# Kernel optimization log

Measured on AMD Instinct MI355X. Metric: run time of the kernel, lower is better.

The kernel has to match this reference:

```python
import jax, jax.numpy as jnp
import numpy as np

B, N, D, H = 8, 2048, 256, 8
HD = D // H  # head_dim = 32
LN_EPS = 1e-5


def setup_inputs() -> dict:
    key = jax.random.key(0)
    ks = jax.random.split(key, 8)
    x = jax.random.normal(ks[0], (B, N, D), dtype=jnp.float32)
    # dense 0/1 adjacency with guaranteed self-loops (avoids all -inf softmax rows)
    adj = jax.random.randint(ks[1], (B, N, N), 0, 2, dtype=jnp.int32)
    adj = jnp.maximum(adj, jnp.eye(N, dtype=jnp.int32)[None, :, :])
    s = 0.02
    Wq = jax.random.normal(ks[2], (D, D), dtype=jnp.float32) * s
    Wk = jax.random.normal(ks[3], (D, D), dtype=jnp.float32) * s
    Wv = jax.random.normal(ks[4], (D, D), dtype=jnp.float32) * s
    Wo = jax.random.normal(ks[5], (D, D), dtype=jnp.float32) * s
    zeros = jnp.zeros((D,), dtype=jnp.float32)
    return {
        "x": x, "adjacency": adj,
        "Wq": Wq, "bq": zeros, "Wk": Wk, "bk": zeros,
        "Wv": Wv, "bv": zeros, "Wo": Wo, "bo": zeros,
        "gamma": jnp.ones((D,), dtype=jnp.float32), "beta": zeros,
    }


def reference(x, adjacency, Wq, bq, Wk, bk, Wv, bv, Wo, bo, gamma, beta):
    b, n, d = x.shape
    q = (x @ Wq + bq).reshape(b, n, H, HD)
    k = (x @ Wk + bk).reshape(b, n, H, HD)
    v = (x @ Wv + bv).reshape(b, n, H, HD)
    # scores: [B, N(query), M(key), H]
    scores = jnp.einsum('bnhd,bmhd->bnmh', q, k) / jnp.sqrt(jnp.float32(HD))
    mask = (adjacency == 0)[..., None]  # [B,N,M,1] broadcasts over heads
    scores = jnp.where(mask, -jnp.inf, scores)
    weights = jax.nn.softmax(scores, axis=2)  # softmax over key axis m
    # dropout is identity in eval mode
    attended = jnp.einsum('bnmh,bmhd->bnhd', weights, v).reshape(b, n, d)
    out = attended @ Wo + bo
    out = out + x  # residual (output.shape == x.shape since input_dim == output_dim)
    mu = jnp.mean(out, axis=-1, keepdims=True)
    var = jnp.mean(jnp.square(out - mu), axis=-1, keepdims=True)
    return (out - mu) * jax.lax.rsqrt(var + LN_EPS) * gamma + beta
```

## Files before the change

### kernel.cpp

```cpp
#include <hip/hip_runtime.h>
#include <hip/hip_bf16.h>
#include <cstdint>
#include <cstddef>

#define B_ 8
#define N_ 2048
#define D_ 256
#define H_ 8
#define HD_ 32
#define LN_EPS 1e-5f
#define QSCALE 0.25506275f

typedef __attribute__((ext_vector_type(8))) short short8;
typedef __attribute__((ext_vector_type(4))) float f32x4;
typedef __attribute__((ext_vector_type(16))) float f32x16;

static __device__ __forceinline__ float exp2v(float x) {
#if __has_builtin(__builtin_amdgcn_exp2f)
    return __builtin_amdgcn_exp2f(x);
#else
    float r;
    asm("v_exp_f32 %0, %1" : "=v"(r) : "v"(x));
    return r;
#endif
}

static __device__ __forceinline__ unsigned short f2bf(float f) {
    union { float f; unsigned int u; } v; v.f = f;
    unsigned int r = v.u + 0x7fffu + ((v.u >> 16) & 1u);
    return (unsigned short)(r >> 16);
}

static __device__ __forceinline__ float bf2f(unsigned short u) {
    union { unsigned int u; float f; } v; v.u = ((unsigned int)u) << 16;
    return v.f;
}

static __device__ __forceinline__ unsigned int cvtpk(float lo, float hi) {
    unsigned int d;
    asm("v_cvt_pk_bf16_f32 %0, %1, %2" : "=v"(d) : "v"(lo), "v"(hi));
    return d;
}

__global__ __launch_bounds__(256) void k_prep_x(const float* __restrict__ x,
                                                unsigned short* __restrict__ xbf, int n4) {
    int i = blockIdx.x * 256 + threadIdx.x;
    if (i >= n4) return;
    float4 v = reinterpret_cast<const float4*>(x)[i];
    ushort4 o;
    o.x = f2bf(v.x); o.y = f2bf(v.y); o.z = f2bf(v.z); o.w = f2bf(v.w);
    reinterpret_cast<ushort4*>(xbf)[i] = o;
}

__global__ __launch_bounds__(256) void k_prep_w(const float* __restrict__ w0, const float* __restrict__ w1,
                                                const float* __restrict__ w2, const float* __restrict__ w3,
                                                unsigned short* __restrict__ wt) {
    int c = blockIdx.x, mat = blockIdx.y, k = threadIdx.x;
    const float* w = (mat == 0) ? w0 : (mat == 1) ? w1 : (mat == 2) ? w2 : w3;
    wt[((size_t)(mat * 256 + c)) * 256 + k] = f2bf(w[k * 256 + c]);
}

__global__ __launch_bounds__(256) void k_mask(const int* __restrict__ adj,
                                              unsigned int* __restrict__ mbg) {
    int wave = (blockIdx.x * 256 + threadIdx.x) >> 6;
    int lane = threadIdx.x & 63;
    int shamt = 4 * (lane & 7);
    int g8 = lane >> 3;
    const int4* p = reinterpret_cast<const int4*>(adj) + (size_t)wave * 1024 + lane;
    unsigned int* outp = mbg + (size_t)wave * 128;

    int4 v[16];
#pragma unroll
    for (int i = 0; i < 16; ++i)
        v[i] = p[i * 64];

#pragma unroll
    for (int i = 0; i < 16; ++i) {
        unsigned int nib = (v[i].x != 0 ? 1u : 0u) | (v[i].y != 0 ? 2u : 0u)
                         | (v[i].z != 0 ? 4u : 0u) | (v[i].w != 0 ? 8u : 0u);
        unsigned int r = nib << shamt;
        r |= (unsigned int)__shfl_xor((int)r, 1, 64);
        r |= (unsigned int)__shfl_xor((int)r, 2, 64);
        r |= (unsigned int)__shfl_xor((int)r, 4, 64);
        if ((lane & 7) == 0) outp[i * 8 + g8] = r;
    }
}

__global__ __launch_bounds__(256) void k_qkv(const unsigned short* __restrict__ xbf,
                                             const unsigned short* __restrict__ wt,
                                             const float* __restrict__ bq, const float* __restrict__ bk,
                                             const float* __restrict__ bv,
                                             unsigned short* __restrict__ Qb, unsigned short* __restrict__ Kb,
                                             unsigned short* __restrict__ Vs) {
    int mat = blockIdx.y;
    int lane = threadIdx.x & 63;
    int wv = threadIdx.x >> 6;
    int row0 = blockIdx.x * 64 + wv * 16;
    int l15 = lane & 15, lg = lane >> 4;
    const float* bias = (mat == 0) ? bq : (mat == 1) ? bk : bv;
    const float qs = (mat == 0) ? QSCALE : 1.0f;
    const unsigned short* wm = wt + (size_t)mat * 65536;

    short8 af[8];
    const unsigned short* xrow = xbf + (size_t)(row0 + l15) * 256 + lg * 8;
#pragma unroll
    for (int kk = 0; kk < 8; ++kk)
        af[kk] = *reinterpret_cast<const short8*>(xrow + kk * 32);

    int b = row0 >> 11;
    int nbase = (row0 & 2047) + lg * 4;

    for (int ci = 0; ci < 16; ++ci) {
        const unsigned short* wrow = wm + (size_t)(ci * 16 + l15) * 256 + lg * 8;
        f32x4 acc = {0.f, 0.f, 0.f, 0.f};
#pragma unroll
        for (int kk = 0; kk < 8; ++kk) {
            short8 bfg = *reinterpret_cast<const short8*>(wrow + kk * 32);
            acc = __builtin_amdgcn_mfma_f32_16x16x32_bf16(af[kk], bfg, acc, 0, 0, 0);
        }
        int col = ci * 16 + l15;
        float bcol = bias[col];
        int h = col >> 5, hd = col & 31;
        if (mat < 2) {
            unsigned short* dst = (mat == 0) ? Qb : Kb;
#pragma unroll
            for (int r = 0; r < 4; ++r) {
                size_t off = ((size_t)(b * 8 + h) * 2048 + nbase + r) * 32 + hd;
                dst[off] = f2bf((acc[r] + bcol) * qs);
            }
        } else {
            size_t off = (size_t)(b * 8 + h) * 65536
                       + ((size_t)(nbase >> 4) * 32 + hd) * 16 + (nbase & 15);
            ushort4 o;
            o.x = f2bf(acc[0] + bcol); o.y = f2bf(acc[1] + bcol);
            o.z = f2bf(acc[2] + bcol); o.w = f2bf(acc[3] + bcol);
            *reinterpret_cast<ushort4*>(Vs + off) = o;
        }
    }
}

__global__ __launch_bounds__(256, 6) void k_attn(const unsigned short* __restrict__ Qb,
                                                 const unsigned short* __restrict__ Kb,
                                                 const unsigned short* __restrict__ Vs,
                                                 const unsigned int* __restrict__ mbg,
                                                 unsigned short* __restrict__ att) {
    __shared__ unsigned int mbits[32][66];
    int tid = threadIdx.x;
    int lane = tid & 63;
    int l31 = lane & 31, hi = lane >> 5;
    int b = blockIdx.x & 7;
    int hg = (blockIdx.x >> 3) & 1;
    int q0 = (blockIdx.x >> 4) * 32;
    int head = hg * 4 + (tid >> 6);

    {
        int row = tid >> 3, c0 = (tid & 7) * 8;
        const unsigned int* src = mbg + ((size_t)(b * N_ + q0 + row)) * 64 + c0;
        uint4 v4 = *reinterpret_cast<const uint4*>(src);
        uint4 w4 = *reinterpret_cast<const uint4*>(src + 4);
        mbits[row][c0 + 0] = v4.x; mbits[row][c0 + 1] = v4.y;
        mbits[row][c0 + 2] = v4.z; mbits[row][c0 + 3] = v4.w;
        mbits[row][c0 + 4] = w4.x; mbits[row][c0 + 5] = w4.y;
        mbits[row][c0 + 6] = w4.z; mbits[row][c0 + 7] = w4.w;
    }
    __syncthreads();

    int bh = b * 8 + head;
    const unsigned short* Qh = Qb + (size_t)bh * N_ * HD_;
    const unsigned short* Kh = Kb + (size_t)bh * N_ * HD_;
    const unsigned short* Vh = Vs + (size_t)bh * 65536;

    short8 qf0 = *reinterpret_cast<const short8*>(Qh + (size_t)(q0 + l31) * HD_ + hi * 8);
    short8 qf1 = *reinterpret_cast<const short8*>(Qh + (size_t)(q0 + l31) * HD_ + hi * 8 + 16);
    const unsigned short* krow = Kh + (size_t)l31 * HD_ + hi * 8;
    const unsigned short* vfp = Vh + (size_t)l31 * 16 + hi * 8;

    const f32x16 fz = {0.f,0.f,0.f,0.f,0.f,0.f,0.f,0.f,0.f,0.f,0.f,0.f,0.f,0.f,0.f,0.f};
    const short8 onesf = {0x3F80, 0x3F80, 0x3F80, 0x3F80, 0x3F80, 0x3F80, 0x3F80, 0x3F80};
    f32x16 attacc = fz;
    f32x16 onesacc = fz;
    const unsigned int* mrow = &mbits[l31][0];

#pragma unroll 2
    for (int m0 = 0; m0 < N_; m0 += 32) {
        short8 kf0 = *reinterpret_cast<const short8*>(krow + (size_t)m0 * HD_);
        short8 kf1 = *reinterpret_cast<const short8*>(krow + (size_t)m0 * HD_ + 16);
        short8 vf0 = *reinterpret_cast<const short8*>(vfp + (size_t)(m0 >> 4) * 512);
        short8 vf1 = *reinterpret_cast<const short8*>(vfp + (size_t)(m0 >> 4) * 512 + 512);
        unsigned int wl = mrow[m0 >> 5] >> (4 * hi);

        __builtin_amdgcn_s_setprio(1);
        f32x16 s = __builtin_amdgcn_mfma_f32_32x32x16_bf16(kf0, qf0, fz, 0, 0, 0);
        s = __builtin_amdgcn_mfma_f32_32x32x16_bf16(kf1, qf1, s, 0, 0, 0);
        __builtin_amdgcn_s_setprio(0);

        unsigned int pd[4][2];
#pragma unroll
        for (int g = 0; g < 4; ++g) {
            unsigned int nib = (wl >> (8 * g)) & 15u;
            float p0 = (nib & 1u) ? exp2v(s[4 * g + 0]) : 0.f;
            float p1 = (nib & 2u) ? exp2v(s[4 * g + 1]) : 0.f;
            float p2 = (nib & 4u) ? exp2v(s[4 * g + 2]) : 0.f;
            float p3 = (nib & 8u) ? exp2v(s[4 * g + 3]) : 0.f;
            pd[g][0] = cvtpk(p0, p1);
            pd[g][1] = cvtpk(p2, p3);
        }
        asm("v_permlane32_swap_b32 %0, %1" : "+v"(pd[0][0]), "+v"(pd[1][0]));
        asm("v_permlane32_swap_b32 %0, %1" : "+v"(pd[0][1]), "+v"(pd[1][1]));
        asm("v_permlane32_swap_b32 %0, %1" : "+v"(pd[2][0]), "+v"(pd[3][0]));
        asm("v_permlane32_swap_b32 %0, %1" : "+v"(pd[2][1]), "+v"(pd[3][1]));

        union { short8 s8; unsigned int u[4]; } bf0, bf1;
        bf0.u[0] = pd[0][0]; bf0.u[1] = pd[0][1]; bf0.u[2] = pd[1][0]; bf0.u[3] = pd[1][1];
        bf1.u[0] = pd[2][0]; bf1.u[1] = pd[2][1]; bf1.u[2] = pd[3][0]; bf1.u[3] = pd[3][1];

        __builtin_amdgcn_s_setprio(1);
        attacc = __builtin_amdgcn_mfma_f32_32x32x16_bf16(vf0, bf0.s8, attacc, 0, 0, 0);
        attacc = __builtin_amdgcn_mfma_f32_32x32x16_bf16(vf1, bf1.s8, attacc, 0, 0, 0);
        onesacc = __builtin_amdgcn_mfma_f32_32x32x16_bf16(onesf, bf0.s8, onesacc, 0, 0, 0);
        onesacc = __builtin_amdgcn_mfma_f32_32x32x16_bf16(onesf, bf1.s8, onesacc, 0, 0, 0);
        __builtin_amdgcn_s_setprio(0);
    }

    float rcp = 1.f / onesacc[0];

    unsigned short* arow = att + ((size_t)b * N_ + q0 + l31) * D_ + head * HD_;
#pragma unroll
    for (int g = 0; g < 4; ++g) {
        ushort4 o;
        o.x = f2bf(attacc[4 * g + 0] * rcp);
        o.y = f2bf(attacc[4 * g + 1] * rcp);
        o.z = f2bf(attacc[4 * g + 2] * rcp);
        o.w = f2bf(attacc[4 * g + 3] * rcp);
        *reinterpret_cast<ushort4*>(arow + 8 * g + 4 * hi) = o;
    }
}

__global__ __launch_bounds__(256) void k_outln(const unsigned short* __restrict__ att,
                                               const unsigned short* __restrict__ wot,
                                               const float* __restrict__ bo,
                                               const unsigned short* __restrict__ xbf,
                                               const float* __restrict__ gamma, const float* __restrict__ beta,
                                               float* __restrict__ out) {
    int lane = threadIdx.x & 63, wv = threadIdx.x >> 6;
    int l15 = lane & 15, lg = lane >> 4;
    int row0 = blockIdx.x * 64 + wv * 16;

    short8 af[8];
    const unsigned short* arow = att + (size_t)(row0 + l15) * 256 + lg * 8;
#pragma unroll
    for (int kk = 0; kk < 8; ++kk)
        af[kk] = *reinterpret_cast<const short8*>(arow + kk * 32);

    float v[16][4];
#pragma unroll
    for (int ci = 0; ci < 16; ++ci) {
        const unsigned short* wrow = wot + (size_t)(ci * 16 + l15) * 256 + lg * 8;
        f32x4 acc = {0.f, 0.f, 0.f, 0.f};
#pragma unroll
        for (int kk = 0; kk < 8; ++kk) {
            short8 bfg = *reinterpret_cast<const short8*>(wrow + kk * 32);
            acc = __builtin_amdgcn_mfma_f32_16x16x32_bf16(af[kk], bfg, acc, 0, 0, 0);
        }
        float bcol = bo[ci * 16 + l15];
#pragma unroll
        for (int r = 0; r < 4; ++r)
            v[ci][r] = acc[r] + bcol + bf2f(xbf[(size_t)(row0 + lg * 4 + r) * 256 + ci * 16 + l15]);
    }

    float sum[4] = {0.f, 0.f, 0.f, 0.f}, sq[4] = {0.f, 0.f, 0.f, 0.f};
#pragma unroll
    for (int ci = 0; ci < 16; ++ci)
#pragma unroll
        for (int r = 0; r < 4; ++r) {
            sum[r] += v[ci][r];
            sq[r] += v[ci][r] * v[ci][r];
        }
#pragma unroll
    for (int d = 1; d < 16; d <<= 1)
#pragma unroll
        for (int r = 0; r < 4; ++r) {
            sum[r] += __shfl_xor(sum[r], d, 64);
            sq[r] += __shfl_xor(sq[r], d, 64);
        }

    float mu[4], rs[4];
#pragma unroll
    for (int r = 0; r < 4; ++r) {
        mu[r] = sum[r] * (1.f / 256.f);
        float var = sq[r] * (1.f / 256.f) - mu[r] * mu[r];
        rs[r] = rsqrtf(var + LN_EPS);
    }

#pragma unroll
    for (int ci = 0; ci < 16; ++ci) {
        float g = gamma[ci * 16 + l15], be = beta[ci * 16 + l15];
#pragma unroll
        for (int r = 0; r < 4; ++r)
            out[(size_t)(row0 + lg * 4 + r) * 256 + ci * 16 + l15] = (v[ci][r] - mu[r]) * rs[r] * g + be;
    }
}

extern "C" void kernel_launch(void* const* d_in, const int* in_sizes, int n_in,
                              void* d_out, int out_size, void* d_ws, size_t ws_size,
                              hipStream_t stream) {
    (void)in_sizes; (void)n_in; (void)out_size; (void)ws_size;
    const float* x     = (const float*)d_in[0];
    const int*   adj   = (const int*)d_in[1];
    const float* Wq    = (const float*)d_in[2];
    const float* bq    = (const float*)d_in[3];
    const float* Wk    = (const float*)d_in[4];
    const float* bk    = (const float*)d_in[5];
    const float* Wv    = (const float*)d_in[6];
    const float* bv    = (const float*)d_in[7];
    const float* Wo    = (const float*)d_in[8];
    const float* bo    = (const float*)d_in[9];
    const float* gamma = (const float*)d_in[10];
    const float* beta  = (const float*)d_in[11];
    float* out = (float*)d_out;

    char* ws = (char*)d_ws;
    unsigned short* xbf = (unsigned short*)ws; ws += (size_t)16384 * 256 * 2;
    unsigned short* wt  = (unsigned short*)ws; ws += (size_t)4 * 256 * 256 * 2;
    unsigned short* Qb  = (unsigned short*)ws; ws += (size_t)B_ * H_ * N_ * HD_ * 2;
    unsigned short* Kb  = (unsigned short*)ws; ws += (size_t)B_ * H_ * N_ * HD_ * 2;
    unsigned short* Vs  = (unsigned short*)ws; ws += (size_t)B_ * H_ * N_ * HD_ * 2;
    unsigned short* att = (unsigned short*)ws; ws += (size_t)16384 * 256 * 2;
    unsigned int*   mbg = (unsigned int*)ws;   ws += (size_t)B_ * N_ * 64 * 4;

    k_prep_x<<<4096, 256, 0, stream>>>(x, xbf, 1048576);
    k_prep_w<<<dim3(256, 4), 256, 0, stream>>>(Wq, Wk, Wv, Wo, wt);
    k_mask<<<2048, 256, 0, stream>>>(adj, mbg);
    k_qkv<<<dim3(256, 3), 256, 0, stream>>>(xbf, wt, bq, bk, bv, Qb, Kb, Vs);
    k_attn<<<1024, 256, 0, stream>>>(Qb, Kb, Vs, mbg, att);
    k_outln<<<256, 256, 0, stream>>>(att, wt + 3 * 65536, bo, xbf, gamma, beta, out);
}
```

Measured before the change: 184.1 us.

## Share K/V tiles across four query waves via double-buffered LDS staging

Attention blocks now cover one (batch, head) with four waves over 128 queries, instead of four heads over 32 queries. Each 32-key K/V tile is loaded cooperatively into a double-buffered LDS buffer and reused by all four waves. K and V are written in a fragment-ready layout so each staging load is contiguous. The mask kernel now emits a transposed bitmask so each wave reads one coalesced word per key tile. The change trades a block-wide barrier every tile and lower occupancy (launch bounds 6 to 4) for fourfold less global K/V traffic. The mask kernel also launches far fewer blocks.

```diff
diff --git a/kernel.cpp b/kernel.cpp
--- a/kernel.cpp
+++ b/kernel.cpp
@@ -60,29 +60,44 @@
     wt[((size_t)(mat * 256 + c)) * 256 + k] = f2bf(w[k * 256 + c]);
 }
 
-__global__ __launch_bounds__(256) void k_mask(const int* __restrict__ adj,
-                                              unsigned int* __restrict__ mbg) {
-    int wave = (blockIdx.x * 256 + threadIdx.x) >> 6;
-    int lane = threadIdx.x & 63;
+__global__ __launch_bounds__(256) void k_maskT(const int* __restrict__ adj,
+                                               unsigned int* __restrict__ mbgT) {
+    __shared__ unsigned int bits[64][65];
+    int tid = threadIdx.x, lane = tid & 63, wv = tid >> 6;
+    int b = blockIdx.x >> 5, rg = blockIdx.x & 31;
+    int r0 = rg * 64;
     int shamt = 4 * (lane & 7);
     int g8 = lane >> 3;
-    const int4* p = reinterpret_cast<const int4*>(adj) + (size_t)wave * 1024 + lane;
-    unsigned int* outp = mbg + (size_t)wave * 128;
-
-    int4 v[16];
-#pragma unroll
-    for (int i = 0; i < 16; ++i)
-        v[i] = p[i * 64];
-
-#pragma unroll
-    for (int i = 0; i < 16; ++i) {
-        unsigned int nib = (v[i].x != 0 ? 1u : 0u) | (v[i].y != 0 ? 2u : 0u)
-                         | (v[i].z != 0 ? 4u : 0u) | (v[i].w != 0 ? 8u : 0u);
-        unsigned int r = nib << shamt;
-        r |= (unsigned int)__shfl_xor((int)r, 1, 64);
-        r |= (unsigned int)__shfl_xor((int)r, 2, 64);
-        r |= (unsigned int)__shfl_xor((int)r, 4, 64);
-        if ((lane & 7) == 0) outp[i * 8 + g8] = r;
+
+#pragma unroll 1
+    for (int p = 0; p < 8; ++p) {
+        int lr0 = p * 8 + wv * 2;
+        const int4* src = reinterpret_cast<const int4*>(adj)
+                        + (size_t)(b * N_ + r0 + lr0) * 512 + lane;
+        int4 v[16];
+#pragma unroll
+        for (int i = 0; i < 16; ++i)
+            v[i] = src[i * 64];
+#pragma unroll
+        for (int i = 0; i < 16; ++i) {
+            unsigned int nib = (v[i].x != 0 ? 1u : 0u) | (v[i].y != 0 ? 2u : 0u)
+                             | (v[i].z != 0 ? 4u : 0u) | (v[i].w != 0 ? 8u : 0u);
+            unsigned int r = nib << shamt;
+            r |= (unsigned int)__shfl_xor((int)r, 1, 64);
+            r |= (unsigned int)__shfl_xor((int)r, 2, 64);
+            r |= (unsigned int)__shfl_xor((int)r, 4, 64);
+            if ((lane & 7) == 0) {
+                int wlin = i * 8 + g8;
+                bits[lr0 + (wlin >> 6)][wlin & 63] = r;
+            }
+        }
+    }
+    __syncthreads();
+
+#pragma unroll
+    for (int j = 0; j < 16; ++j) {
+        int w = wv + 4 * j;
+        mbgT[((size_t)(b * 64 + w)) * N_ + r0 + lane] = bits[lane][w];
     }
 }
 
@@ -90,7 +105,7 @@
                                              const unsigned short* __restrict__ wt,
                                              const float* __restrict__ bq, const float* __restrict__ bk,
                                              const float* __restrict__ bv,
-                                             unsigned short* __restrict__ Qb, unsigned short* __restrict__ Kb,
+                                             unsigned short* __restrict__ Qb, unsigned short* __restrict__ Ks,
                                              unsigned short* __restrict__ Vs) {
     int mat = blockIdx.y;
     int lane = threadIdx.x & 63;
@@ -121,16 +136,23 @@
         int col = ci * 16 + l15;
         float bcol = bias[col];
         int h = col >> 5, hd = col & 31;
-        if (mat < 2) {
-            unsigned short* dst = (mat == 0) ? Qb : Kb;
+        size_t bh64 = (size_t)(b * 8 + h) * 65536;
+        if (mat == 0) {
+#pragma unroll
+            for (int r = 0; r < 4; ++r)
+                Qb[bh64 + (size_t)(nbase + r) * 32 + hd] = f2bf((acc[r] + bcol) * qs);
+        } else if (mat == 1) {
 #pragma unroll
             for (int r = 0; r < 4; ++r) {
-                size_t off = ((size_t)(b * 8 + h) * 2048 + nbase + r) * 32 + hd;
-                dst[off] = f2bf((acc[r] + bcol) * qs);
+                int n = nbase + r;
+                size_t off = bh64 + (size_t)(n >> 5) * 1024 + (hd >> 4) * 512
+                           + (((hd >> 3) & 1) * 32 + (n & 31)) * 8 + (hd & 7);
+                Ks[off] = f2bf(acc[r] + bcol);
             }
         } else {
-            size_t off = (size_t)(b * 8 + h) * 65536
-                       + ((size_t)(nbase >> 4) * 32 + hd) * 16 + (nbase & 15);
+            int posb = nbase & 31;
+            size_t off = bh64 + (size_t)(nbase >> 5) * 1024 + (posb >> 4) * 512
+                       + ((((posb >> 3) & 1) * 32 + hd)) * 8 + (posb & 7);
             ushort4 o;
             o.x = f2bf(acc[0] + bcol); o.y = f2bf(acc[1] + bcol);
             o.z = f2bf(acc[2] + bcol); o.w = f2bf(acc[3] + bcol);
@@ -139,55 +161,57 @@
     }
 }
 
-__global__ __launch_bounds__(256, 6) void k_attn(const unsigned short* __restrict__ Qb,
-                                                 const unsigned short* __restrict__ Kb,
+__global__ __launch_bounds__(256, 4) void k_attn(const unsigned short* __restrict__ Qb,
+                                                 const unsigned short* __restrict__ Ks,
                                                  const unsigned short* __restrict__ Vs,
-                                                 const unsigned int* __restrict__ mbg,
+                                                 const unsigned int* __restrict__ mbgT,
                                                  unsigned short* __restrict__ att) {
-    __shared__ unsigned int mbits[32][66];
+    __shared__ unsigned short kv[2][2048];
     int tid = threadIdx.x;
-    int lane = tid & 63;
+    int lane = tid & 63, wv = tid >> 6;
     int l31 = lane & 31, hi = lane >> 5;
     int b = blockIdx.x & 7;
-    int hg = (blockIdx.x >> 3) & 1;
-    int q0 = (blockIdx.x >> 4) * 32;
-    int head = hg * 4 + (tid >> 6);
-
-    {
-        int row = tid >> 3, c0 = (tid & 7) * 8;
-        const unsigned int* src = mbg + ((size_t)(b * N_ + q0 + row)) * 64 + c0;
-        uint4 v4 = *reinterpret_cast<const uint4*>(src);
-        uint4 w4 = *reinterpret_cast<const uint4*>(src + 4);
-        mbits[row][c0 + 0] = v4.x; mbits[row][c0 + 1] = v4.y;
-        mbits[row][c0 + 2] = v4.z; mbits[row][c0 + 3] = v4.w;
-        mbits[row][c0 + 4] = w4.x; mbits[row][c0 + 5] = w4.y;
-        mbits[row][c0 + 6] = w4.z; mbits[row][c0 + 7] = w4.w;
-    }
-    __syncthreads();
-
-    int bh = b * 8 + head;
-    const unsigned short* Qh = Qb + (size_t)bh * N_ * HD_;
-    const unsigned short* Kh = Kb + (size_t)bh * N_ * HD_;
-    const unsigned short* Vh = Vs + (size_t)bh * 65536;
+    int h = (blockIdx.x >> 3) & 7;
+    int qc = blockIdx.x >> 6;
+    int q0 = qc * 128 + wv * 32;
+    int bh = b * 8 + h;
+
+    const unsigned short* gK = Ks + (size_t)bh * 65536;
+    const unsigned short* gV = Vs + (size_t)bh * 65536;
+    const unsigned short* gstage = (wv < 2 ? gK : gV) + (size_t)(wv & 1) * 512 + (size_t)lane * 8;
+    const unsigned short* Qh = Qb + (size_t)bh * 65536;
+    const unsigned int* mbase = mbgT + (size_t)b * 131072 + q0 + l31;
 
     short8 qf0 = *reinterpret_cast<const short8*>(Qh + (size_t)(q0 + l31) * HD_ + hi * 8);
     short8 qf1 = *reinterpret_cast<const short8*>(Qh + (size_t)(q0 + l31) * HD_ + hi * 8 + 16);
-    const unsigned short* krow = Kh + (size_t)l31 * HD_ + hi * 8;
-    const unsigned short* vfp = Vh + (size_t)l31 * 16 + hi * 8;
+
+    {
+        short8 t0 = *reinterpret_cast<const short8*>(gstage);
+        *reinterpret_cast<short8*>(&kv[0][wv * 512 + lane * 8]) = t0;
+    }
+    unsigned int mw = mbase[0];
+    __syncthreads();
 
     const f32x16 fz = {0.f,0.f,0.f,0.f,0.f,0.f,0.f,0.f,0.f,0.f,0.f,0.f,0.f,0.f,0.f,0.f};
     const short8 onesf = {0x3F80, 0x3F80, 0x3F80, 0x3F80, 0x3F80, 0x3F80, 0x3F80, 0x3F80};
     f32x16 attacc = fz;
     f32x16 onesacc = fz;
-    const unsigned int* mrow = &mbits[l31][0];
-
-#pragma unroll 2
-    for (int m0 = 0; m0 < N_; m0 += 32) {
-        short8 kf0 = *reinterpret_cast<const short8*>(krow + (size_t)m0 * HD_);
-        short8 kf1 = *reinterpret_cast<const short8*>(krow + (size_t)m0 * HD_ + 16);
-        short8 vf0 = *reinterpret_cast<const short8*>(vfp + (size_t)(m0 >> 4) * 512);
-        short8 vf1 = *reinterpret_cast<const short8*>(vfp + (size_t)(m0 >> 4) * 512 + 512);
-        unsigned int wl = mrow[m0 >> 5] >> (4 * hi);
+
+#pragma unroll 1
+    for (int t = 0; t < 64; ++t) {
+        int cur = t & 1;
+        short8 tmpn = {};
+        unsigned int mwn = 0;
+        if (t < 63) {
+            tmpn = *reinterpret_cast<const short8*>(gstage + (size_t)(t + 1) * 1024);
+            mwn = mbase[(size_t)(t + 1) * 2048];
+        }
+
+        short8 kf0 = *reinterpret_cast<const short8*>(&kv[cur][lane * 8]);
+        short8 kf1 = *reinterpret_cast<const short8*>(&kv[cur][512 + lane * 8]);
+        short8 vf0 = *reinterpret_cast<const short8*>(&kv[cur][1024 + lane * 8]);
+        short8 vf1 = *reinterpret_cast<const short8*>(&kv[cur][1536 + lane * 8]);
+        unsigned int wl = mw >> (4 * hi);
 
         __builtin_amdgcn_s_setprio(1);
         f32x16 s = __builtin_amdgcn_mfma_f32_32x32x16_bf16(kf0, qf0, fz, 0, 0, 0);
@@ -220,11 +244,17 @@
         onesacc = __builtin_amdgcn_mfma_f32_32x32x16_bf16(onesf, bf0.s8, onesacc, 0, 0, 0);
         onesacc = __builtin_amdgcn_mfma_f32_32x32x16_bf16(onesf, bf1.s8, onesacc, 0, 0, 0);
         __builtin_amdgcn_s_setprio(0);
+
+        if (t < 63) {
+            *reinterpret_cast<short8*>(&kv[cur ^ 1][wv * 512 + lane * 8]) = tmpn;
+            mw = mwn;
+        }
+        __syncthreads();
     }
 
     float rcp = 1.f / onesacc[0];
 
-    unsigned short* arow = att + ((size_t)b * N_ + q0 + l31) * D_ + head * HD_;
+    unsigned short* arow = att + ((size_t)b * N_ + q0 + l31) * D_ + h * HD_;
 #pragma unroll
     for (int g = 0; g < 4; ++g) {
         ushort4 o;
@@ -323,15 +353,15 @@
     unsigned short* xbf = (unsigned short*)ws; ws += (size_t)16384 * 256 * 2;
     unsigned short* wt  = (unsigned short*)ws; ws += (size_t)4 * 256 * 256 * 2;
     unsigned short* Qb  = (unsigned short*)ws; ws += (size_t)B_ * H_ * N_ * HD_ * 2;
-    unsigned short* Kb  = (unsigned short*)ws; ws += (size_t)B_ * H_ * N_ * HD_ * 2;
+    unsigned short* Ks  = (unsigned short*)ws; ws += (size_t)B_ * H_ * N_ * HD_ * 2;
     unsigned short* Vs  = (unsigned short*)ws; ws += (size_t)B_ * H_ * N_ * HD_ * 2;
     unsigned short* att = (unsigned short*)ws; ws += (size_t)16384 * 256 * 2;
-    unsigned int*   mbg = (unsigned int*)ws;   ws += (size_t)B_ * N_ * 64 * 4;
+    unsigned int*   mbgT = (unsigned int*)ws;  ws += (size_t)B_ * 64 * N_ * 4;
 
     k_prep_x<<<4096, 256, 0, stream>>>(x, xbf, 1048576);
     k_prep_w<<<dim3(256, 4), 256, 0, stream>>>(Wq, Wk, Wv, Wo, wt);
-    k_mask<<<2048, 256, 0, stream>>>(adj, mbg);
-    k_qkv<<<dim3(256, 3), 256, 0, stream>>>(xbf, wt, bq, bk, bv, Qb, Kb, Vs);
-    k_attn<<<1024, 256, 0, stream>>>(Qb, Kb, Vs, mbg, att);
+    k_maskT<<<256, 256, 0, stream>>>(adj, mbgT);
+    k_qkv<<<dim3(256, 3), 256, 0, stream>>>(xbf, wt, bq, bk, bv, Qb, Ks, Vs);
+    k_attn<<<1024, 256, 0, stream>>>(Qb, Ks, Vs, mbgT, att);
     k_outln<<<256, 256, 0, stream>>>(att, wt + 3 * 65536, bo, xbf, gamma, beta, out);
 }
```

After: 192.6 us. +4.6%, slower.

## Pre-swizzle K and V into MFMA fragment order and mask via LUT AND

Applied to the files above, without the earlier changes.

The QKV projection now writes K and V in a per-32-key tile layout that matches the MFMA operand fragments. Each lane in the attention loop can then load contiguous 16-byte chunks at lane*8 offsets, which makes global loads fully coalesced. The masking step changes from per-element conditional exp to computing exp unconditionally, then ANDing packed bf16 pairs with masks taken from a 16-entry shared-memory LUT. This removes branches and selects, at the cost of extra LDS lookups and always evaluating exp.

```diff
diff --git a/kernel.cpp b/kernel.cpp
--- a/kernel.cpp
+++ b/kernel.cpp
@@ -90,7 +90,7 @@
                                              const unsigned short* __restrict__ wt,
                                              const float* __restrict__ bq, const float* __restrict__ bk,
                                              const float* __restrict__ bv,
-                                             unsigned short* __restrict__ Qb, unsigned short* __restrict__ Kb,
+                                             unsigned short* __restrict__ Qb, unsigned short* __restrict__ Ks,
                                              unsigned short* __restrict__ Vs) {
     int mat = blockIdx.y;
     int lane = threadIdx.x & 63;
@@ -121,16 +121,23 @@
         int col = ci * 16 + l15;
         float bcol = bias[col];
         int h = col >> 5, hd = col & 31;
-        if (mat < 2) {
-            unsigned short* dst = (mat == 0) ? Qb : Kb;
+        size_t bh64 = (size_t)(b * 8 + h) * 65536;
+        if (mat == 0) {
+#pragma unroll
+            for (int r = 0; r < 4; ++r)
+                Qb[bh64 + (size_t)(nbase + r) * 32 + hd] = f2bf((acc[r] + bcol) * qs);
+        } else if (mat == 1) {
 #pragma unroll
             for (int r = 0; r < 4; ++r) {
-                size_t off = ((size_t)(b * 8 + h) * 2048 + nbase + r) * 32 + hd;
-                dst[off] = f2bf((acc[r] + bcol) * qs);
+                int n = nbase + r;
+                size_t off = bh64 + (size_t)(n >> 5) * 1024 + (hd >> 4) * 512
+                           + (((hd >> 3) & 1) * 32 + (n & 31)) * 8 + (hd & 7);
+                Ks[off] = f2bf(acc[r] + bcol);
             }
         } else {
-            size_t off = (size_t)(b * 8 + h) * 65536
-                       + ((size_t)(nbase >> 4) * 32 + hd) * 16 + (nbase & 15);
+            int posb = nbase & 31;
+            size_t off = bh64 + (size_t)(nbase >> 5) * 1024 + (posb >> 4) * 512
+                       + ((((posb >> 3) & 1) * 32 + hd)) * 8 + (posb & 7);
             ushort4 o;
             o.x = f2bf(acc[0] + bcol); o.y = f2bf(acc[1] + bcol);
             o.z = f2bf(acc[2] + bcol); o.w = f2bf(acc[3] + bcol);
@@ -140,18 +147,20 @@
 }
 
 __global__ __launch_bounds__(256, 6) void k_attn(const unsigned short* __restrict__ Qb,
-                                                 const unsigned short* __restrict__ Kb,
+                                                 const unsigned short* __restrict__ Ks,
                                                  const unsigned short* __restrict__ Vs,
                                                  const unsigned int* __restrict__ mbg,
                                                  unsigned short* __restrict__ att) {
     __shared__ unsigned int mbits[32][66];
+    __shared__ uint2 lut16[16];
     int tid = threadIdx.x;
-    int lane = tid & 63;
+    int lane = tid & 63, wv = tid >> 6;
     int l31 = lane & 31, hi = lane >> 5;
     int b = blockIdx.x & 7;
     int hg = (blockIdx.x >> 3) & 1;
     int q0 = (blockIdx.x >> 4) * 32;
-    int head = hg * 4 + (tid >> 6);
+    int head = hg * 4 + wv;
+    int bh = b * 8 + head;
 
     {
         int row = tid >> 3, c0 = (tid & 7) * 8;
@@ -162,49 +171,56 @@
         mbits[row][c0 + 2] = v4.z; mbits[row][c0 + 3] = v4.w;
         mbits[row][c0 + 4] = w4.x; mbits[row][c0 + 5] = w4.y;
         mbits[row][c0 + 6] = w4.z; mbits[row][c0 + 7] = w4.w;
+        if (tid < 16) {
+            uint2 e;
+            e.x = (tid & 1 ? 0xFFFFu : 0u) | (tid & 2 ? 0xFFFF0000u : 0u);
+            e.y = (tid & 4 ? 0xFFFFu : 0u) | (tid & 8 ? 0xFFFF0000u : 0u);
+            lut16[tid] = e;
+        }
     }
     __syncthreads();
 
-    int bh = b * 8 + head;
-    const unsigned short* Qh = Qb + (size_t)bh * N_ * HD_;
-    const unsigned short* Kh = Kb + (size_t)bh * N_ * HD_;
-    const unsigned short* Vh = Vs + (size_t)bh * 65536;
-
-    short8 qf0 = *reinterpret_cast<const short8*>(Qh + (size_t)(q0 + l31) * HD_ + hi * 8);
-    short8 qf1 = *reinterpret_cast<const short8*>(Qh + (size_t)(q0 + l31) * HD_ + hi * 8 + 16);
-    const unsigned short* krow = Kh + (size_t)l31 * HD_ + hi * 8;
-    const unsigned short* vfp = Vh + (size_t)l31 * 16 + hi * 8;
+    const unsigned short* gK = Ks + (size_t)bh * 65536 + (size_t)lane * 8;
+    const unsigned short* gV = Vs + (size_t)bh * 65536 + (size_t)lane * 8;
+    const unsigned short* Qh = Qb + (size_t)bh * 65536;
+    const unsigned int* mrow = &mbits[l31][0];
+
+    short8 qf0 = *reinterpret_cast<const short8*>(Qh + (size_t)(q0 + l31) * 32 + hi * 8);
+    short8 qf1 = *reinterpret_cast<const short8*>(Qh + (size_t)(q0 + l31) * 32 + hi * 8 + 16);
 
     const f32x16 fz = {0.f,0.f,0.f,0.f,0.f,0.f,0.f,0.f,0.f,0.f,0.f,0.f,0.f,0.f,0.f,0.f};
     const short8 onesf = {0x3F80, 0x3F80, 0x3F80, 0x3F80, 0x3F80, 0x3F80, 0x3F80, 0x3F80};
     f32x16 attacc = fz;
     f32x16 onesacc = fz;
-    const unsigned int* mrow = &mbits[l31][0];
 
 #pragma unroll 2
-    for (int m0 = 0; m0 < N_; m0 += 32) {
-        short8 kf0 = *reinterpret_cast<const short8*>(krow + (size_t)m0 * HD_);
-        short8 kf1 = *reinterpret_cast<const short8*>(krow + (size_t)m0 * HD_ + 16);
-        short8 vf0 = *reinterpret_cast<const short8*>(vfp + (size_t)(m0 >> 4) * 512);
-        short8 vf1 = *reinterpret_cast<const short8*>(vfp + (size_t)(m0 >> 4) * 512 + 512);
-        unsigned int wl = mrow[m0 >> 5] >> (4 * hi);
+    for (int t = 0; t < 64; ++t) {
+        short8 kf0 = *reinterpret_cast<const short8*>(gK + (size_t)t * 1024);
+        short8 kf1 = *reinterpret_cast<const short8*>(gK + (size_t)t * 1024 + 512);
+        short8 vf0 = *reinterpret_cast<const short8*>(gV + (size_t)t * 1024);
+        short8 vf1 = *reinterpret_cast<const short8*>(gV + (size_t)t * 1024 + 512);
+        unsigned int wl = mrow[t] >> (4 * hi);
 
         __builtin_amdgcn_s_setprio(1);
         f32x16 s = __builtin_amdgcn_mfma_f32_32x32x16_bf16(kf0, qf0, fz, 0, 0, 0);
         s = __builtin_amdgcn_mfma_f32_32x32x16_bf16(kf1, qf1, s, 0, 0, 0);
         __builtin_amdgcn_s_setprio(0);
 
+        uint2 m0 = lut16[wl & 15u];
+        uint2 m1 = lut16[(wl >> 8) & 15u];
+        uint2 m2 = lut16[(wl >> 16) & 15u];
+        uint2 m3 = lut16[(wl >> 24) & 15u];
+
         unsigned int pd[4][2];
-#pragma unroll
-        for (int g = 0; g < 4; ++g) {
-            unsigned int nib = (wl >> (8 * g)) & 15u;
-            float p0 = (nib & 1u) ? exp2v(s[4 * g + 0]) : 0.f;
-            float p1 = (nib & 2u) ? exp2v(s[4 * g + 1]) : 0.f;
-            float p2 = (nib & 4u) ? exp2v(s[4 * g + 2]) : 0.f;
-            float p3 = (nib & 8u) ? exp2v(s[4 * g + 3]) : 0.f;
-            pd[g][0] = cvtpk(p0, p1);
-            pd[g][1] = cvtpk(p2, p3);
-        }
+        pd[0][0] = cvtpk(exp2v(s[0]),  exp2v(s[1]))  & m0.x;
+        pd[0][1] = cvtpk(exp2v(s[2]),  exp2v(s[3]))  & m0.y;
+        pd[1][0] = cvtpk(exp2v(s[4]),  exp2v(s[5]))  & m1.x;
+        pd[1][1] = cvtpk(exp2v(s[6]),  exp2v(s[7]))  & m1.y;
+        pd[2][0] = cvtpk(exp2v(s[8]),  exp2v(s[9]))  & m2.x;
+        pd[2][1] = cvtpk(exp2v(s[10]), exp2v(s[11])) & m2.y;
+        pd[3][0] = cvtpk(exp2v(s[12]), exp2v(s[13])) & m3.x;
+        pd[3][1] = cvtpk(exp2v(s[14]), exp2v(s[15])) & m3.y;
+
         asm("v_permlane32_swap_b32 %0, %1" : "+v"(pd[0][0]), "+v"(pd[1][0]));
         asm("v_permlane32_swap_b32 %0, %1" : "+v"(pd[0][1]), "+v"(pd[1][1]));
         asm("v_permlane32_swap_b32 %0, %1" : "+v"(pd[2][0]), "+v"(pd[3][0]));
@@ -323,7 +339,7 @@
     unsigned short* xbf = (unsigned short*)ws; ws += (size_t)16384 * 256 * 2;
     unsigned short* wt  = (unsigned short*)ws; ws += (size_t)4 * 256 * 256 * 2;
     unsigned short* Qb  = (unsigned short*)ws; ws += (size_t)B_ * H_ * N_ * HD_ * 2;
-    unsigned short* Kb  = (unsigned short*)ws; ws += (size_t)B_ * H_ * N_ * HD_ * 2;
+    unsigned short* Ks  = (unsigned short*)ws; ws += (size_t)B_ * H_ * N_ * HD_ * 2;
     unsigned short* Vs  = (unsigned short*)ws; ws += (size_t)B_ * H_ * N_ * HD_ * 2;
     unsigned short* att = (unsigned short*)ws; ws += (size_t)16384 * 256 * 2;
     unsigned int*   mbg = (unsigned int*)ws;   ws += (size_t)B_ * N_ * 64 * 4;
@@ -331,7 +347,7 @@
     k_prep_x<<<4096, 256, 0, stream>>>(x, xbf, 1048576);
     k_prep_w<<<dim3(256, 4), 256, 0, stream>>>(Wq, Wk, Wv, Wo, wt);
     k_mask<<<2048, 256, 0, stream>>>(adj, mbg);
-    k_qkv<<<dim3(256, 3), 256, 0, stream>>>(xbf, wt, bq, bk, bv, Qb, Kb, Vs);
-    k_attn<<<1024, 256, 0, stream>>>(Qb, Kb, Vs, mbg, att);
+    k_qkv<<<dim3(256, 3), 256, 0, stream>>>(xbf, wt, bq, bk, bv, Qb, Ks, Vs);
+    k_attn<<<1024, 256, 0, stream>>>(Qb, Ks, Vs, mbg, att);
     k_outln<<<256, 256, 0, stream>>>(att, wt + 3 * 65536, bo, xbf, gamma, beta, out);
 }
```

After: 193.0 us. +4.8%, slower.
